# Performance work log

Hardware: AMD Instinct MI355X
Metric: run time of the kernel (lower is better)

Reference implementation:

```python
import math
import jax, jax.numpy as jnp
import numpy as np

B, N, D = 8, 1024, 1024
H, TKQ, TV = 16, 64, 64
DOUT = H * TV  # 1024, equals D
EPS = 1e-5


def _layer_norm(x, g, b):
    mu = jnp.mean(x, axis=-1, keepdims=True)
    var = jnp.mean((x - mu) ** 2, axis=-1, keepdims=True)
    return (x - mu) * jax.lax.rsqrt(var + EPS) * g + b


def setup_inputs() -> dict:
    key = jax.random.key(0)
    ks = jax.random.split(key, 16)
    s_w = 1.0 / math.sqrt(D)
    inp = {
        "tokens": jax.random.normal(ks[0], (B, N, D), jnp.float32),
        "Wq": jax.random.normal(ks[1], (H, D, TKQ), jnp.float32) * s_w,
        "bq": jax.random.uniform(ks[2], (H, 1, TKQ), jnp.float32, -s_w, s_w),
        "Wk": jax.random.normal(ks[3], (H, D, TKQ), jnp.float32) * s_w,
        "bk": jax.random.uniform(ks[4], (H, 1, TKQ), jnp.float32, -s_w, s_w),
        "Wv": jax.random.normal(ks[5], (H, D, TV), jnp.float32) * s_w,
        "bv": jax.random.uniform(ks[6], (H, 1, TV), jnp.float32, -s_w, s_w),
        "W1": jax.random.normal(ks[7], (DOUT, DOUT), jnp.float32) * (1.0 / math.sqrt(DOUT)),
        "b1": jax.random.uniform(ks[8], (DOUT,), jnp.float32, -s_w, s_w),
        "W2": jax.random.normal(ks[9], (DOUT, DOUT), jnp.float32) * (1.0 / math.sqrt(DOUT)),
        "b2": jax.random.uniform(ks[10], (DOUT,), jnp.float32, -s_w, s_w),
        "g1": jnp.ones((DOUT,), jnp.float32),
        "be1": jnp.zeros((DOUT,), jnp.float32),
        "g2": jnp.ones((DOUT,), jnp.float32),
        "be2": jnp.zeros((DOUT,), jnp.float32),
    }
    return inp


def reference(tokens, Wq, bq, Wk, bk, Wv, bv, W1, b1, W2, b2, g1, be1, g2, be2):
    # per-head projections: tokens[:,None] @ W + b  -> [B,H,N,T]
    tq = jnp.einsum("bnd,hdt->bhnt", tokens, Wq) + bq
    tk = jnp.einsum("bnd,hdt->bhnt", tokens, Wk) + bk
    tv = jnp.einsum("bnd,hdt->bhnt", tokens, Wv) + bv
    # non-standard scale: sqrt(num_heads * dim_tv)
    scale = math.sqrt(H * TV)
    scores = jnp.einsum("bhqt,bhkt->bhqk", tq, tk) / scale
    attn = jax.nn.softmax(scores, axis=-1)
    out = jnp.einsum("bhqk,bhkt->bhqt", attn, tv)  # [B,H,N,TV]
    # original flatten order: (B,N,TV,H) -> reshape(B,N,TV*H)
    out = jnp.transpose(out, (0, 2, 3, 1)).reshape(B, N, TV * H)
    # post-LN SAB path
    h = out + tokens
    h = _layer_norm(h, g1, be1)
    ff = jax.nn.relu(h @ W1 + b1) @ W2 + b2
    h = h + ff
    return _layer_norm(h, g2, be2)
```

## Files before the change

### kernel.cpp

```cpp
#include <hip/hip_runtime.h>
#include <hip/hip_bf16.h>

#define BB 8
#define NN_ 1024
#define DD 1024
#define HH 16
#define TT_ 64
#define MM (BB * NN_)

typedef __attribute__((ext_vector_type(8))) short short8;
typedef __attribute__((ext_vector_type(4))) float f32x4;
typedef __attribute__((ext_vector_type(4))) unsigned int u32x4;

__device__ __forceinline__ void g2lds16(const void* g, void* l) {
    __builtin_amdgcn_global_load_lds(
        (const __attribute__((address_space(1))) void*)g,
        (__attribute__((address_space(3))) void*)l, 16, 0, 0);
}

__device__ __forceinline__ __hip_bfloat16 f2b(float x) { return __float2bfloat16(x); }
__device__ __forceinline__ float b2f(unsigned short u) {
    unsigned v = (unsigned)u << 16;
    return __builtin_bit_cast(float, v);
}

__device__ __forceinline__ unsigned cvtpk(float a, float b) {
    unsigned r;
    asm("v_cvt_pk_bf16_f32 %0, %1, %2" : "=v"(r) : "v"(a), "v"(b));
    return r;
}

__device__ __forceinline__ int xcd_swz(int bid, int nwg) {
    return (bid & 7) * (nwg >> 3) + (bid >> 3);
}

__global__ __launch_bounds__(256) void k_cvt_tokens(const float* __restrict__ in,
                                                    __hip_bfloat16* __restrict__ out) {
    int i = (blockIdx.x * 256 + threadIdx.x) * 4;
    float4 v = *(const float4*)&in[i];
    out[i + 0] = f2b(v.x); out[i + 1] = f2b(v.y);
    out[i + 2] = f2b(v.z); out[i + 3] = f2b(v.w);
}

__global__ __launch_bounds__(256) void k_cvt_wqkv(const float* __restrict__ Wq,
                                                  const float* __restrict__ Wk,
                                                  const float* __restrict__ Wv,
                                                  __hip_bfloat16* __restrict__ out) {
    __shared__ float tile[64][65];
    const int bid = blockIdx.x;
    const int proj = bid >> 8, h = (bid >> 4) & 15, dt = bid & 15;
    const float* W = proj == 0 ? Wq : (proj == 1 ? Wk : Wv);
    const float* src = W + ((size_t)h * 1024 + dt * 64) * 64;
    const int c = threadIdx.x & 63, r0 = threadIdx.x >> 6;
#pragma unroll
    for (int p = 0; p < 16; p++) {
        const int r = p * 4 + r0;
        tile[r][c] = src[(size_t)r * 64 + c];
    }
    __syncthreads();
    __hip_bfloat16* dst = out + (size_t)(proj * 1024 + h * 64) * 1024 + dt * 64;
#pragma unroll
    for (int p = 0; p < 16; p++) {
        const int r = p * 4 + r0;
        dst[(size_t)r * 1024 + c] = f2b(tile[c][r]);
    }
}

__global__ __launch_bounds__(256) void k_cvt_w2(const float* __restrict__ W1,
                                                const float* __restrict__ W2,
                                                __hip_bfloat16* __restrict__ o1,
                                                __hip_bfloat16* __restrict__ o2) {
    __shared__ float tile[64][65];
    const int which = blockIdx.x >> 8, b = blockIdx.x & 255;
    const float* W = which ? W2 : W1;
    __hip_bfloat16* out = which ? o2 : o1;
    const int ct = b & 15, dt = b >> 4;
    const float* src = W + (size_t)(dt * 64) * 1024 + ct * 64;
    const int c = threadIdx.x & 63, r0 = threadIdx.x >> 6;
#pragma unroll
    for (int p = 0; p < 16; p++) {
        const int r = p * 4 + r0;
        tile[r][c] = src[(size_t)r * 1024 + c];
    }
    __syncthreads();
    __hip_bfloat16* dst = out + (size_t)(ct * 64) * 1024 + dt * 64;
#pragma unroll
    for (int p = 0; p < 16; p++) {
        const int r = p * 4 + r0;
        dst[(size_t)r * 1024 + c] = f2b(tile[c][r]);
    }
}

template <int MODE>
__global__ __launch_bounds__(512) void k_gemm(
    const __hip_bfloat16* __restrict__ A, const __hip_bfloat16* __restrict__ Bt,
    const float* __restrict__ bias0, const float* __restrict__ bias1,
    const float* __restrict__ bias2,
    __hip_bfloat16* __restrict__ ob0, __hip_bfloat16* __restrict__ ob1,
    __hip_bfloat16* __restrict__ ob2,
    const __hip_bfloat16* __restrict__ res) {
    __shared__ __align__(16) __hip_bfloat16 As[2][128 * 64];
    __shared__ __align__(16) __hip_bfloat16 Bs[2][128 * 64];

    const int tid = threadIdx.x;
    const int wid = tid >> 6, lane = tid & 63;
    const int l15 = lane & 15, lhi = lane >> 4;
    const int wm = wid >> 1, wn = wid & 1;

    const int nbx = gridDim.x;
    int bid = xcd_swz(blockIdx.y * nbx + blockIdx.x, nbx * gridDim.y);
    const int n0 = (bid % nbx) * 128, m0 = (bid / nbx) * 128;

    const int srow = lane >> 3;
    const int scol = ((lane & 7) ^ srow) * 8;

    const __hip_bfloat16* gsrc;
    if (wid < 4)
        gsrc = A + (size_t)(m0 + wid * 32 + srow) * 1024 + scol;
    else
        gsrc = Bt + (size_t)(n0 + (wid - 4) * 32 + srow) * 1024 + scol;
    const int lofs = (wid & 3) * 2048;

    auto stage = [&](int kt, int bufi) {
        __hip_bfloat16* lb = (wid < 4) ? &As[bufi][lofs] : &Bs[bufi][lofs];
#pragma unroll
        for (int i = 0; i < 4; ++i)
            g2lds16(gsrc + kt * 64 + (size_t)i * 8 * 1024, lb + i * 512);
    };

    f32x4 acc[2][4];
#pragma unroll
    for (int i = 0; i < 2; i++)
#pragma unroll
        for (int j = 0; j < 4; j++) acc[i][j] = (f32x4){0.f, 0.f, 0.f, 0.f};

    stage(0, 0);
    const int swz = l15 & 7;

    for (int kt = 0; kt < 16; ++kt) {
        const int cur = kt & 1;
        if (kt < 15) {
            stage(kt + 1, cur ^ 1);
            asm volatile("s_waitcnt vmcnt(4)" ::: "memory");
        } else {
            asm volatile("s_waitcnt vmcnt(0)" ::: "memory");
        }
        __builtin_amdgcn_s_barrier();
        asm volatile("" ::: "memory");
        __builtin_amdgcn_s_setprio(1);
#pragma unroll
        for (int kk = 0; kk < 2; ++kk) {
            const int ch = ((kk * 4 + lhi) ^ swz) * 8;
            short8 af[2], bfr[4];
#pragma unroll
            for (int mi = 0; mi < 2; mi++)
                af[mi] = *(const short8*)&As[cur][(wm * 32 + mi * 16 + l15) * 64 + ch];
#pragma unroll
            for (int ni = 0; ni < 4; ni++)
                bfr[ni] = *(const short8*)&Bs[cur][(wn * 64 + ni * 16 + l15) * 64 + ch];
#pragma unroll
            for (int mi = 0; mi < 2; mi++)
#pragma unroll
                for (int ni = 0; ni < 4; ni++)
                    acc[mi][ni] = __builtin_amdgcn_mfma_f32_16x16x32_bf16(
                        af[mi], bfr[ni], acc[mi][ni], 0, 0, 0);
        }
        __builtin_amdgcn_s_setprio(0);
        asm volatile("" ::: "memory");
        __builtin_amdgcn_s_barrier();
    }

#pragma unroll
    for (int mi = 0; mi < 2; mi++) {
#pragma unroll
        for (int ni = 0; ni < 4; ni++) {
            const int col = n0 + wn * 64 + ni * 16 + l15;
#pragma unroll
            for (int r = 0; r < 4; r++) {
                const int m = m0 + wm * 32 + mi * 16 + lhi * 4 + r;
                float v = acc[mi][ni][r];
                if (MODE == 0) {
                    const int proj = col >> 10, hh = (col >> 6) & 15, t = col & 63;
                    const float* bp = proj == 0 ? bias0 : (proj == 1 ? bias1 : bias2);
                    v += bp[hh * 64 + t];
                    const int b = m >> 10, n = m & 1023;
                    if (proj == 0)
                        ob0[((size_t)(b * 16 + hh) * 1024 + n) * 64 + t] = f2b(v * 0.04508422f);
                    else if (proj == 1)
                        ob1[((size_t)(b * 16 + hh) * 1024 + n) * 64 + t] = f2b(v);
                    else
                        ob2[((size_t)(b * 16 + hh) * 64 + t) * 1024 + n] = f2b(v);
                } else if (MODE == 1) {
                    v += bias0[col];
                    ob0[(size_t)m * 1024 + col] = f2b(fmaxf(v, 0.f));
                } else {
                    v += bias0[col] + b2f(*(const unsigned short*)&res[(size_t)m * 1024 + col]);
                    ob0[(size_t)m * 1024 + col] = f2b(v);
                }
            }
        }
    }
}

__global__ __launch_bounds__(512) void k_attn(const __hip_bfloat16* __restrict__ Q,
                                              const __hip_bfloat16* __restrict__ Kg,
                                              const __hip_bfloat16* __restrict__ Vt,
                                              __hip_bfloat16* __restrict__ attn_out) {
    __shared__ __align__(16) __hip_bfloat16 Ks[2][2][64 * 64];
    __shared__ __align__(16) __hip_bfloat16 Vs[2][2][64 * 64];

    const int tid = threadIdx.x, wid = tid >> 6, lane = tid & 63;
    const int l15 = lane & 15, lhi = lane >> 4;
    const int bid = xcd_swz(blockIdx.x, gridDim.x);
    const int qb = bid & 3, head = (bid >> 2) & 15, b = bid >> 6;
    const int bh = b * 16 + head;
    const __hip_bfloat16* Qg = Q + ((size_t)bh * 1024 + qb * 256) * 64;
    const __hip_bfloat16* Kp = Kg + (size_t)bh * 1024 * 64;
    const __hip_bfloat16* Vp = Vt + (size_t)bh * 64 * 1024;
    const int srow = lane >> 3;
    const int scol = ((lane & 7) ^ srow) * 8;

    auto stageKV = [&](int t, int bufi) {
        const int krow = wid * 8 + srow;
        const int kperm = (krow & 0x23) | ((krow & 0x0C) << 1) | ((krow & 0x10) >> 2);
#pragma unroll
        for (int h = 0; h < 2; h++) {
            g2lds16(Kp + (size_t)(t * 128 + h * 64 + kperm) * 64 + scol, &Ks[bufi][h][wid * 512]);
            g2lds16(Vp + (size_t)krow * 1024 + t * 128 + h * 64 + scol, &Vs[bufi][h][wid * 512]);
        }
    };

    short8 qf[2][2];
#pragma unroll
    for (int g = 0; g < 2; g++)
#pragma unroll
        for (int c = 0; c < 2; c++)
            qf[g][c] = *(const short8*)&Qg[(size_t)(wid * 32 + g * 16 + l15) * 64 + c * 32 + lhi * 8];

    stageKV(0, 0);

    f32x4 o[2][4];
#pragma unroll
    for (int g = 0; g < 2; g++)
#pragma unroll
        for (int i = 0; i < 4; i++) o[g][i] = (f32x4){0.f, 0.f, 0.f, 0.f};
    f32x4 lacc[2] = {(f32x4){0.f, 0.f, 0.f, 0.f}, (f32x4){0.f, 0.f, 0.f, 0.f}};
    const short bf16_one = (short)0x3F80;
    const short8 ones = (short8){bf16_one, bf16_one, bf16_one, bf16_one,
                                 bf16_one, bf16_one, bf16_one, bf16_one};

    const int sw = l15 & 7;
    const int c0 = (lhi ^ sw) * 8;

    for (int t = 0; t < 8; ++t) {
        const int cur = t & 1;
        if (t < 7) {
            stageKV(t + 1, cur ^ 1);
            asm volatile("s_waitcnt vmcnt(4)" ::: "memory");
        } else {
            asm volatile("s_waitcnt vmcnt(0)" ::: "memory");
        }
        __builtin_amdgcn_s_barrier();
        asm volatile("" ::: "memory");

#pragma unroll
        for (int h = 0; h < 2; h++) {
            const __hip_bfloat16* Kc = &Ks[cur][h][0];
            const __hip_bfloat16* Vc = &Vs[cur][h][0];

            f32x4 s[2][4];
            __builtin_amdgcn_s_setprio(1);
#pragma unroll
            for (int nt = 0; nt < 4; ++nt) {
                const int kr = (nt * 16 + l15) * 64;
                short8 k0 = *(const short8*)&Kc[kr + c0];
                short8 k1 = *(const short8*)&Kc[kr + (c0 ^ 32)];
#pragma unroll
                for (int g = 0; g < 2; g++) {
                    f32x4 z = (f32x4){0.f, 0.f, 0.f, 0.f};
                    z = __builtin_amdgcn_mfma_f32_16x16x32_bf16(k0, qf[g][0], z, 0, 0, 0);
                    s[g][nt] = __builtin_amdgcn_mfma_f32_16x16x32_bf16(k1, qf[g][1], z, 0, 0, 0);
                }
            }
            __builtin_amdgcn_s_setprio(0);

#pragma unroll
            for (int g = 0; g < 2; g++)
#pragma unroll
                for (int nt = 0; nt < 4; nt++)
#pragma unroll
                    for (int r = 0; r < 4; r++) s[g][nt][r] = __builtin_exp2f(s[g][nt][r]);

            short8 pf[2][2];
#pragma unroll
            for (int g = 0; g < 2; g++) {
                u32x4 w0 = (u32x4){cvtpk(s[g][0][0], s[g][0][1]), cvtpk(s[g][0][2], s[g][0][3]),
                                   cvtpk(s[g][1][0], s[g][1][1]), cvtpk(s[g][1][2], s[g][1][3])};
                u32x4 w1 = (u32x4){cvtpk(s[g][2][0], s[g][2][1]), cvtpk(s[g][2][2], s[g][2][3]),
                                   cvtpk(s[g][3][0], s[g][3][1]), cvtpk(s[g][3][2], s[g][3][3])};
                pf[g][0] = __builtin_bit_cast(short8, w0);
                pf[g][1] = __builtin_bit_cast(short8, w1);
            }

            __builtin_amdgcn_s_setprio(1);
#pragma unroll
            for (int g = 0; g < 2; g++) {
                lacc[g] = __builtin_amdgcn_mfma_f32_16x16x32_bf16(pf[g][0], ones, lacc[g], 0, 0, 0);
                lacc[g] = __builtin_amdgcn_mfma_f32_16x16x32_bf16(pf[g][1], ones, lacc[g], 0, 0, 0);
            }
#pragma unroll
            for (int tt = 0; tt < 4; tt++) {
                const int vr = (tt * 16 + l15) * 64;
                short8 v0 = *(const short8*)&Vc[vr + c0];
                short8 v1 = *(const short8*)&Vc[vr + (c0 ^ 32)];
#pragma unroll
                for (int g = 0; g < 2; g++) {
                    o[g][tt] = __builtin_amdgcn_mfma_f32_16x16x32_bf16(pf[g][0], v0, o[g][tt], 0, 0, 0);
                    o[g][tt] = __builtin_amdgcn_mfma_f32_16x16x32_bf16(pf[g][1], v1, o[g][tt], 0, 0, 0);
                }
            }
            __builtin_amdgcn_s_setprio(0);
        }
        asm volatile("" ::: "memory");
        __builtin_amdgcn_s_barrier();
    }

#pragma unroll
    for (int g = 0; g < 2; g++)
#pragma unroll
        for (int r = 0; r < 4; r++) {
            const float inv_r = 1.f / lacc[g][r];
            const int row = qb * 256 + wid * 32 + g * 16 + lhi * 4 + r;
#pragma unroll
            for (int tt = 0; tt < 4; tt++) {
                const int ch = (tt * 16 + l15) * 16 + head;
                attn_out[((size_t)(b * 1024 + row)) * 1024 + ch] = f2b(o[g][tt][r] * inv_r);
            }
        }
}

__global__ __launch_bounds__(256) void k_ln1(const __hip_bfloat16* __restrict__ x1,
                                             const __hip_bfloat16* __restrict__ x2,
                                             const float* __restrict__ g,
                                             const float* __restrict__ be,
                                             __hip_bfloat16* __restrict__ y) {
    const int row = blockIdx.x;
    const int tid = threadIdx.x, wid = tid >> 6, lane = tid & 63;
    const int c = tid * 4;
    const ushort4 u = *(const ushort4*)&x1[(size_t)row * 1024 + c];
    const ushort4 u2 = *(const ushort4*)&x2[(size_t)row * 1024 + c];
    float4 xv;
    xv.x = b2f(u.x) + b2f(u2.x);
    xv.y = b2f(u.y) + b2f(u2.y);
    xv.z = b2f(u.z) + b2f(u2.z);
    xv.w = b2f(u.w) + b2f(u2.w);
    float s = xv.x + xv.y + xv.z + xv.w;
    float q = xv.x * xv.x + xv.y * xv.y + xv.z * xv.z + xv.w * xv.w;
#pragma unroll
    for (int msk = 1; msk < 64; msk <<= 1) {
        s += __shfl_xor(s, msk);
        q += __shfl_xor(q, msk);
    }
    __shared__ float ss[4], qq[4];
    if (lane == 0) { ss[wid] = s; qq[wid] = q; }
    __syncthreads();
    s = ss[0] + ss[1] + ss[2] + ss[3];
    q = qq[0] + qq[1] + qq[2] + qq[3];
    const float mu = s * (1.f / 1024.f);
    const float var = q * (1.f / 1024.f) - mu * mu;
    const float rs = rsqrtf(var + 1e-5f);
    float4 gv = *(const float4*)&g[c];
    float4 bv = *(const float4*)&be[c];
    __hip_bfloat16* d = y + (size_t)row * 1024 + c;
    d[0] = f2b((xv.x - mu) * rs * gv.x + bv.x);
    d[1] = f2b((xv.y - mu) * rs * gv.y + bv.y);
    d[2] = f2b((xv.z - mu) * rs * gv.z + bv.z);
    d[3] = f2b((xv.w - mu) * rs * gv.w + bv.w);
}

__global__ __launch_bounds__(256) void k_ln2(const __hip_bfloat16* __restrict__ x,
                                             const float* __restrict__ g,
                                             const float* __restrict__ be,
                                             float* __restrict__ y) {
    const int row = blockIdx.x;
    const int tid = threadIdx.x, wid = tid >> 6, lane = tid & 63;
    const int c = tid * 4;
    const ushort4 u = *(const ushort4*)&x[(size_t)row * 1024 + c];
    float4 xv;
    xv.x = b2f(u.x); xv.y = b2f(u.y); xv.z = b2f(u.z); xv.w = b2f(u.w);
    float s = xv.x + xv.y + xv.z + xv.w;
    float q = xv.x * xv.x + xv.y * xv.y + xv.z * xv.z + xv.w * xv.w;
#pragma unroll
    for (int msk = 1; msk < 64; msk <<= 1) {
        s += __shfl_xor(s, msk);
        q += __shfl_xor(q, msk);
    }
    __shared__ float ss[4], qq[4];
    if (lane == 0) { ss[wid] = s; qq[wid] = q; }
    __syncthreads();
    s = ss[0] + ss[1] + ss[2] + ss[3];
    q = qq[0] + qq[1] + qq[2] + qq[3];
    const float mu = s * (1.f / 1024.f);
    const float var = q * (1.f / 1024.f) - mu * mu;
    const float rs = rsqrtf(var + 1e-5f);
    float4 gv = *(const float4*)&g[c];
    float4 bv = *(const float4*)&be[c];
    float4 yv;
    yv.x = (xv.x - mu) * rs * gv.x + bv.x;
    yv.y = (xv.y - mu) * rs * gv.y + bv.y;
    yv.z = (xv.z - mu) * rs * gv.z + bv.z;
    yv.w = (xv.w - mu) * rs * gv.w + bv.w;
    *(float4*)&y[(size_t)row * 1024 + c] = yv;
}

extern "C" void kernel_launch(void* const* d_in, const int* in_sizes, int n_in,
                              void* d_out, int out_size, void* d_ws, size_t ws_size,
                              hipStream_t stream) {
    const float* tokens = (const float*)d_in[0];
    const float* Wq  = (const float*)d_in[1];
    const float* bq  = (const float*)d_in[2];
    const float* Wk  = (const float*)d_in[3];
    const float* bk  = (const float*)d_in[4];
    const float* Wv  = (const float*)d_in[5];
    const float* bv  = (const float*)d_in[6];
    const float* W1  = (const float*)d_in[7];
    const float* b1  = (const float*)d_in[8];
    const float* W2  = (const float*)d_in[9];
    const float* b2  = (const float*)d_in[10];
    const float* g1  = (const float*)d_in[11];
    const float* be1 = (const float*)d_in[12];
    const float* g2  = (const float*)d_in[13];
    const float* be2 = (const float*)d_in[14];

    char* ws = (char*)d_ws;
    const size_t MB = 1024 * 1024;
    __hip_bfloat16* tok_b  = (__hip_bfloat16*)(ws + 0);
    __hip_bfloat16* Wqkv_t = (__hip_bfloat16*)(ws + 16 * MB);
    __hip_bfloat16* W1t    = (__hip_bfloat16*)(ws + 22 * MB);
    __hip_bfloat16* W2t    = (__hip_bfloat16*)(ws + 24 * MB);
    __hip_bfloat16* Qb     = (__hip_bfloat16*)(ws + 26 * MB);
    __hip_bfloat16* Kb     = (__hip_bfloat16*)(ws + 42 * MB);
    __hip_bfloat16* Vtb    = (__hip_bfloat16*)(ws + 58 * MB);
    __hip_bfloat16* attn_b = (__hip_bfloat16*)(ws + 74 * MB);
    __hip_bfloat16* h1     = (__hip_bfloat16*)(ws + 90 * MB);
    __hip_bfloat16* t1     = (__hip_bfloat16*)(ws + 26 * MB);
    __hip_bfloat16* h2     = (__hip_bfloat16*)(ws + 42 * MB);

    k_cvt_tokens<<<8192, 256, 0, stream>>>(tokens, tok_b);
    k_cvt_wqkv<<<768, 256, 0, stream>>>(Wq, Wk, Wv, Wqkv_t);
    k_cvt_w2<<<512, 256, 0, stream>>>(W1, W2, W1t, W2t);

    k_gemm<0><<<dim3(24, 64), 512, 0, stream>>>(tok_b, Wqkv_t, bq, bk, bv,
                                                Qb, Kb, Vtb, nullptr);
    k_attn<<<512, 512, 0, stream>>>(Qb, Kb, Vtb, attn_b);
    k_ln1<<<8192, 256, 0, stream>>>(attn_b, tok_b, g1, be1, h1);
    k_gemm<1><<<dim3(8, 64), 512, 0, stream>>>(h1, W1t, b1, nullptr, nullptr,
                                               t1, nullptr, nullptr, nullptr);
    k_gemm<2><<<dim3(8, 64), 512, 0, stream>>>(t1, W2t, b2, nullptr, nullptr,
                                               h2, nullptr, nullptr, h1);
    k_ln2<<<8192, 256, 0, stream>>>(h2, g2, be2, (float*)d_out);
}
```

Baseline: 223.0 us.

## Merge conversion kernels into one launch and restructure attention score/softmax loop

Combines the three fp32-to-bf16 conversion/transpose kernels into a single k_prep launch with block-range dispatch, removing two kernel launches and their tail gaps. In the attention kernel, the QK^T MFMAs for both K half-tiles now issue back-to-back before the exp/convert and PV phases, giving the scheduler more independent MFMA work to overlap. Launch bounds now request 4 blocks per CU minimum, which constrains register allocation and could cause spills given the larger live score arrays.

```diff
diff --git a/kernel.cpp b/kernel.cpp
--- a/kernel.cpp
+++ b/kernel.cpp
@@ -34,49 +34,51 @@
     return (bid & 7) * (nwg >> 3) + (bid >> 3);
 }
 
-__global__ __launch_bounds__(256) void k_cvt_tokens(const float* __restrict__ in,
-                                                    __hip_bfloat16* __restrict__ out) {
-    int i = (blockIdx.x * 256 + threadIdx.x) * 4;
-    float4 v = *(const float4*)&in[i];
-    out[i + 0] = f2b(v.x); out[i + 1] = f2b(v.y);
-    out[i + 2] = f2b(v.z); out[i + 3] = f2b(v.w);
-}
-
-__global__ __launch_bounds__(256) void k_cvt_wqkv(const float* __restrict__ Wq,
-                                                  const float* __restrict__ Wk,
-                                                  const float* __restrict__ Wv,
-                                                  __hip_bfloat16* __restrict__ out) {
+__global__ __launch_bounds__(256) void k_prep(const float* __restrict__ tokens,
+                                              const float* __restrict__ Wq,
+                                              const float* __restrict__ Wk,
+                                              const float* __restrict__ Wv,
+                                              const float* __restrict__ W1,
+                                              const float* __restrict__ W2,
+                                              __hip_bfloat16* __restrict__ tok_b,
+                                              __hip_bfloat16* __restrict__ Wqkv_t,
+                                              __hip_bfloat16* __restrict__ W1t,
+                                              __hip_bfloat16* __restrict__ W2t) {
     __shared__ float tile[64][65];
     const int bid = blockIdx.x;
-    const int proj = bid >> 8, h = (bid >> 4) & 15, dt = bid & 15;
-    const float* W = proj == 0 ? Wq : (proj == 1 ? Wk : Wv);
-    const float* src = W + ((size_t)h * 1024 + dt * 64) * 64;
+    if (bid < 8192) {
+        int i = (bid * 256 + threadIdx.x) * 4;
+        float4 v = *(const float4*)&tokens[i];
+        tok_b[i + 0] = f2b(v.x); tok_b[i + 1] = f2b(v.y);
+        tok_b[i + 2] = f2b(v.z); tok_b[i + 3] = f2b(v.w);
+        return;
+    }
     const int c = threadIdx.x & 63, r0 = threadIdx.x >> 6;
-#pragma unroll
-    for (int p = 0; p < 16; p++) {
-        const int r = p * 4 + r0;
-        tile[r][c] = src[(size_t)r * 64 + c];
-    }
-    __syncthreads();
-    __hip_bfloat16* dst = out + (size_t)(proj * 1024 + h * 64) * 1024 + dt * 64;
-#pragma unroll
-    for (int p = 0; p < 16; p++) {
-        const int r = p * 4 + r0;
-        dst[(size_t)r * 1024 + c] = f2b(tile[c][r]);
-    }
-}
-
-__global__ __launch_bounds__(256) void k_cvt_w2(const float* __restrict__ W1,
-                                                const float* __restrict__ W2,
-                                                __hip_bfloat16* __restrict__ o1,
-                                                __hip_bfloat16* __restrict__ o2) {
-    __shared__ float tile[64][65];
-    const int which = blockIdx.x >> 8, b = blockIdx.x & 255;
+    if (bid < 8960) {
+        const int q = bid - 8192;
+        const int proj = q >> 8, h = (q >> 4) & 15, dt = q & 15;
+        const float* W = proj == 0 ? Wq : (proj == 1 ? Wk : Wv);
+        const float* src = W + ((size_t)h * 1024 + dt * 64) * 64;
+#pragma unroll
+        for (int p = 0; p < 16; p++) {
+            const int r = p * 4 + r0;
+            tile[r][c] = src[(size_t)r * 64 + c];
+        }
+        __syncthreads();
+        __hip_bfloat16* dst = Wqkv_t + (size_t)(proj * 1024 + h * 64) * 1024 + dt * 64;
+#pragma unroll
+        for (int p = 0; p < 16; p++) {
+            const int r = p * 4 + r0;
+            dst[(size_t)r * 1024 + c] = f2b(tile[c][r]);
+        }
+        return;
+    }
+    const int q = bid - 8960;
+    const int which = q >> 8, b = q & 255;
     const float* W = which ? W2 : W1;
-    __hip_bfloat16* out = which ? o2 : o1;
+    __hip_bfloat16* out = which ? W2t : W1t;
     const int ct = b & 15, dt = b >> 4;
     const float* src = W + (size_t)(dt * 64) * 1024 + ct * 64;
-    const int c = threadIdx.x & 63, r0 = threadIdx.x >> 6;
 #pragma unroll
     for (int p = 0; p < 16; p++) {
         const int r = p * 4 + r0;
@@ -202,10 +204,10 @@
     }
 }
 
-__global__ __launch_bounds__(512) void k_attn(const __hip_bfloat16* __restrict__ Q,
-                                              const __hip_bfloat16* __restrict__ Kg,
-                                              const __hip_bfloat16* __restrict__ Vt,
-                                              __hip_bfloat16* __restrict__ attn_out) {
+__global__ __launch_bounds__(512, 4) void k_attn(const __hip_bfloat16* __restrict__ Q,
+                                                 const __hip_bfloat16* __restrict__ Kg,
+                                                 const __hip_bfloat16* __restrict__ Vt,
+                                                 __hip_bfloat16* __restrict__ attn_out) {
     __shared__ __align__(16) __hip_bfloat16 Ks[2][2][64 * 64];
     __shared__ __align__(16) __hip_bfloat16 Vs[2][2][64 * 64];
 
@@ -263,13 +265,11 @@
         __builtin_amdgcn_s_barrier();
         asm volatile("" ::: "memory");
 
+        f32x4 s[2][2][4];
+        __builtin_amdgcn_s_setprio(1);
 #pragma unroll
         for (int h = 0; h < 2; h++) {
             const __hip_bfloat16* Kc = &Ks[cur][h][0];
-            const __hip_bfloat16* Vc = &Vs[cur][h][0];
-
-            f32x4 s[2][4];
-            __builtin_amdgcn_s_setprio(1);
 #pragma unroll
             for (int nt = 0; nt < 4; ++nt) {
                 const int kr = (nt * 16 + l15) * 64;
@@ -279,34 +279,37 @@
                 for (int g = 0; g < 2; g++) {
                     f32x4 z = (f32x4){0.f, 0.f, 0.f, 0.f};
                     z = __builtin_amdgcn_mfma_f32_16x16x32_bf16(k0, qf[g][0], z, 0, 0, 0);
-                    s[g][nt] = __builtin_amdgcn_mfma_f32_16x16x32_bf16(k1, qf[g][1], z, 0, 0, 0);
+                    s[h][g][nt] = __builtin_amdgcn_mfma_f32_16x16x32_bf16(k1, qf[g][1], z, 0, 0, 0);
                 }
             }
-            __builtin_amdgcn_s_setprio(0);
-
+        }
+        __builtin_amdgcn_s_setprio(0);
+
+        short8 pf[2][2][2];
+#pragma unroll
+        for (int h = 0; h < 2; h++) {
 #pragma unroll
             for (int g = 0; g < 2; g++)
 #pragma unroll
                 for (int nt = 0; nt < 4; nt++)
 #pragma unroll
-                    for (int r = 0; r < 4; r++) s[g][nt][r] = __builtin_exp2f(s[g][nt][r]);
-
-            short8 pf[2][2];
+                    for (int r = 0; r < 4; r++) s[h][g][nt][r] = __builtin_exp2f(s[h][g][nt][r]);
 #pragma unroll
             for (int g = 0; g < 2; g++) {
-                u32x4 w0 = (u32x4){cvtpk(s[g][0][0], s[g][0][1]), cvtpk(s[g][0][2], s[g][0][3]),
-                                   cvtpk(s[g][1][0], s[g][1][1]), cvtpk(s[g][1][2], s[g][1][3])};
-                u32x4 w1 = (u32x4){cvtpk(s[g][2][0], s[g][2][1]), cvtpk(s[g][2][2], s[g][2][3]),
-                                   cvtpk(s[g][3][0], s[g][3][1]), cvtpk(s[g][3][2], s[g][3][3])};
-                pf[g][0] = __builtin_bit_cast(short8, w0);
-                pf[g][1] = __builtin_bit_cast(short8, w1);
-            }
-
+                u32x4 w0 = (u32x4){cvtpk(s[h][g][0][0], s[h][g][0][1]), cvtpk(s[h][g][0][2], s[h][g][0][3]),
+                                   cvtpk(s[h][g][1][0], s[h][g][1][1]), cvtpk(s[h][g][1][2], s[h][g][1][3])};
+                u32x4 w1 = (u32x4){cvtpk(s[h][g][2][0], s[h][g][2][1]), cvtpk(s[h][g][2][2], s[h][g][2][3]),
+                                   cvtpk(s[h][g][3][0], s[h][g][3][1]), cvtpk(s[h][g][3][2], s[h][g][3][3])};
+                pf[h][g][0] = __builtin_bit_cast(short8, w0);
+                pf[h][g][1] = __builtin_bit_cast(short8, w1);
+            }
+
+            const __hip_bfloat16* Vc = &Vs[cur][h][0];
             __builtin_amdgcn_s_setprio(1);
 #pragma unroll
             for (int g = 0; g < 2; g++) {
-                lacc[g] = __builtin_amdgcn_mfma_f32_16x16x32_bf16(pf[g][0], ones, lacc[g], 0, 0, 0);
-                lacc[g] = __builtin_amdgcn_mfma_f32_16x16x32_bf16(pf[g][1], ones, lacc[g], 0, 0, 0);
+                lacc[g] = __builtin_amdgcn_mfma_f32_16x16x32_bf16(pf[h][g][0], ones, lacc[g], 0, 0, 0);
+                lacc[g] = __builtin_amdgcn_mfma_f32_16x16x32_bf16(pf[h][g][1], ones, lacc[g], 0, 0, 0);
             }
 #pragma unroll
             for (int tt = 0; tt < 4; tt++) {
@@ -315,8 +318,8 @@
                 short8 v1 = *(const short8*)&Vc[vr + (c0 ^ 32)];
 #pragma unroll
                 for (int g = 0; g < 2; g++) {
-                    o[g][tt] = __builtin_amdgcn_mfma_f32_16x16x32_bf16(pf[g][0], v0, o[g][tt], 0, 0, 0);
-                    o[g][tt] = __builtin_amdgcn_mfma_f32_16x16x32_bf16(pf[g][1], v1, o[g][tt], 0, 0, 0);
+                    o[g][tt] = __builtin_amdgcn_mfma_f32_16x16x32_bf16(pf[h][g][0], v0, o[g][tt], 0, 0, 0);
+                    o[g][tt] = __builtin_amdgcn_mfma_f32_16x16x32_bf16(pf[h][g][1], v1, o[g][tt], 0, 0, 0);
                 }
             }
             __builtin_amdgcn_s_setprio(0);
@@ -446,9 +449,8 @@
     __hip_bfloat16* t1     = (__hip_bfloat16*)(ws + 26 * MB);
     __hip_bfloat16* h2     = (__hip_bfloat16*)(ws + 42 * MB);
 
-    k_cvt_tokens<<<8192, 256, 0, stream>>>(tokens, tok_b);
-    k_cvt_wqkv<<<768, 256, 0, stream>>>(Wq, Wk, Wv, Wqkv_t);
-    k_cvt_w2<<<512, 256, 0, stream>>>(W1, W2, W1t, W2t);
+    k_prep<<<9472, 256, 0, stream>>>(tokens, Wq, Wk, Wv, W1, W2,
+                                     tok_b, Wqkv_t, W1t, W2t);
 
     k_gemm<0><<<dim3(24, 64), 512, 0, stream>>>(tok_b, Wqkv_t, bq, bk, bv,
                                                 Qb, Kb, Vtb, nullptr);
```

After: 235.0 us. 5.4% more time.
